# Performance work log

Hardware: AMD Instinct MI355X
Metric: run time of the kernel (lower is better)

The kernel has to match this reference:

```python
import jax, jax.numpy as jnp
import numpy as np

H = 2048          # hidden_size
E = 8             # num_experts
TOPK = 2          # num_experts_per_tok
I = 1408          # moe_intermediate_size
IS = 5632         # shared_expert_intermediate_size


def setup_inputs() -> dict:
    key = jax.random.key(0)
    ks = jax.random.split(key, 10)
    s = 0.02
    return {
        "hidden_states": jax.random.normal(ks[0], (2, 512, H), dtype=jnp.float32),
        "gate_w": jax.random.normal(ks[1], (H, E), dtype=jnp.float32) * s,
        "wg": jax.random.normal(ks[2], (E, H, I), dtype=jnp.float32) * s,
        "wu": jax.random.normal(ks[3], (E, H, I), dtype=jnp.float32) * s,
        "wd": jax.random.normal(ks[4], (E, I, H), dtype=jnp.float32) * s,
        "sg": jax.random.normal(ks[5], (H, IS), dtype=jnp.float32) * s,
        "su": jax.random.normal(ks[6], (H, IS), dtype=jnp.float32) * s,
        "sd": jax.random.normal(ks[7], (IS, H), dtype=jnp.float32) * s,
        "shared_gate_w": jax.random.normal(ks[8], (H, 1), dtype=jnp.float32) * s,
    }


def reference(hidden_states, gate_w, wg, wu, wd, sg, su, sd, shared_gate_w):
    B, S, Hd = hidden_states.shape
    x = hidden_states.reshape(-1, Hd)                       # [T, H]
    # Router (softmax in fp32, as in the torch code)
    router_logits = x @ gate_w                              # [T, E]
    probs = jax.nn.softmax(router_logits.astype(jnp.float32), axis=-1)
    rw, sel = jax.lax.top_k(probs, TOPK)                    # [T, K]
    # norm_topk_prob = False -> no renormalization
    rw = rw.astype(x.dtype)
    # Dense combine weights: w[t,e] = sum_k rw[t,k] * 1[sel[t,k]==e]
    combine = (jax.nn.one_hot(sel, E, dtype=x.dtype) * rw[..., None]).sum(axis=1)  # [T, E]
    # Per-expert SwiGLU MLP over all tokens, zero-weighted where unselected
    g = jnp.einsum('th,ehi->eti', x, wg)                    # [E, T, I]
    u = jnp.einsum('th,ehi->eti', x, wu)                    # [E, T, I]
    y = jnp.einsum('eti,eih->eth', jax.nn.silu(g) * u, wd)  # [E, T, H]
    moe_out = jnp.einsum('eth,te->th', y, combine)          # [T, H]
    # Shared expert with sigmoid gate
    shared = (jax.nn.silu(x @ sg) * (x @ su)) @ sd          # [T, H]
    shared = jax.nn.sigmoid(x @ shared_gate_w) * shared     # [T, H]
    final = moe_out + shared
    return final.reshape(B, S, Hd), router_logits
```

## Files before the change

kernel.cpp:

```cpp
#include <hip/hip_runtime.h>
#include <cstdint>
#include <cstddef>

#define Tn 1024
#define Hn 2048
#define En 8
#define In 1408
#define ISn 5632

typedef __attribute__((ext_vector_type(8))) short bf16x8;
typedef __attribute__((ext_vector_type(4))) float f32x4;

__device__ __forceinline__ unsigned short f2bf(float f) {
  unsigned u = __builtin_bit_cast(unsigned, f);
  u += 0x7fffu + ((u >> 16) & 1u);
  return (unsigned short)(u >> 16);
}

#define PK2(a, b) ((unsigned)f2bf(a) | ((unsigned)f2bf(b) << 16))
#define SWZ(row, bir) (((row) << 7) | ((((bir) >> 4) ^ ((row) & 7)) << 4) | ((bir) & 15))

__global__ void router_kernel(const float* __restrict__ x, const float* __restrict__ gw,
                              const float* __restrict__ sgw, float* __restrict__ logits_out,
                              float* __restrict__ combine, float* __restrict__ sgate) {
  int t = blockIdx.x;
  int l = threadIdx.x;
  const float* xr = x + (size_t)t * Hn;
  float acc[En];
#pragma unroll
  for (int e = 0; e < En; ++e) acc[e] = 0.f;
  float accs = 0.f;
  for (int h = l; h < Hn; h += 64) {
    float xv = xr[h];
    const float4 g0 = *(const float4*)(gw + (size_t)h * En);
    const float4 g1 = *(const float4*)(gw + (size_t)h * En + 4);
    acc[0] += xv * g0.x; acc[1] += xv * g0.y; acc[2] += xv * g0.z; acc[3] += xv * g0.w;
    acc[4] += xv * g1.x; acc[5] += xv * g1.y; acc[6] += xv * g1.z; acc[7] += xv * g1.w;
    accs += xv * sgw[h];
  }
#pragma unroll
  for (int e = 0; e < En; ++e) {
#pragma unroll
    for (int off = 32; off > 0; off >>= 1) acc[e] += __shfl_down(acc[e], off);
  }
#pragma unroll
  for (int off = 32; off > 0; off >>= 1) accs += __shfl_down(accs, off);
  if (l == 0) {
    float mx = acc[0];
#pragma unroll
    for (int e = 1; e < En; ++e) mx = fmaxf(mx, acc[e]);
    float p[En], s = 0.f;
#pragma unroll
    for (int e = 0; e < En; ++e) { p[e] = expf(acc[e] - mx); s += p[e]; }
    float inv = 1.f / s;
#pragma unroll
    for (int e = 0; e < En; ++e) p[e] *= inv;
    int i1 = 0;
#pragma unroll
    for (int e = 1; e < En; ++e) if (p[e] > p[i1]) i1 = e;
    int i2 = (i1 == 0) ? 1 : 0;
#pragma unroll
    for (int e = 0; e < En; ++e) if (e != i1 && p[e] > p[i2]) i2 = e;
#pragma unroll
    for (int e = 0; e < En; ++e)
      combine[t * En + e] = (e == i1 || e == i2) ? p[e] : 0.f;
    sgate[t] = 1.f / (1.f + expf(-accs));
#pragma unroll
    for (int e = 0; e < En; ++e) logits_out[t * En + e] = acc[e];
  }
}

__global__ void cvt_x_kernel(const float* __restrict__ x, unsigned short* __restrict__ xb) {
  int i = (blockIdx.x * 256 + threadIdx.x) << 2;
  float4 v = *(const float4*)(x + i);
  ushort4 o;
  o.x = f2bf(v.x); o.y = f2bf(v.y); o.z = f2bf(v.z); o.w = f2bf(v.w);
  *(ushort4*)(xb + i) = o;
}

__device__ __forceinline__ void stage_b(char* sB, const float* __restrict__ src, int ldb, int tid) {
  const int kb = tid >> 5;
  const int nb = tid & 31;
  const float* p = src + (size_t)(kb * 8) * ldb + nb * 4;
  float4 r0 = *(const float4*)p; p += ldb;
  float4 r1 = *(const float4*)p; p += ldb;
  float4 r2 = *(const float4*)p; p += ldb;
  float4 r3 = *(const float4*)p; p += ldb;
  float4 r4 = *(const float4*)p; p += ldb;
  float4 r5 = *(const float4*)p; p += ldb;
  float4 r6 = *(const float4*)p; p += ldb;
  float4 r7 = *(const float4*)p;
  uint4 pk;
  int n, off;
#define STORE_ROW(J, F)                                                        \
  n = nb * 4 + (J);                                                            \
  pk.x = PK2(r0.F, r1.F); pk.y = PK2(r2.F, r3.F);                              \
  pk.z = PK2(r4.F, r5.F); pk.w = PK2(r6.F, r7.F);                              \
  off = (n << 7) | (((kb ^ (n & 7)) << 4));                                    \
  *(uint4*)(sB + off) = pk;
  STORE_ROW(0, x)
  STORE_ROW(1, y)
  STORE_ROW(2, z)
  STORE_ROW(3, w)
#undef STORE_ROW
}

__global__ __launch_bounds__(256, 2)
void gateup_kernel(const unsigned short* __restrict__ xb,
                   const float* __restrict__ Wg, const float* __restrict__ Wu,
                   const float* __restrict__ combine, const float* __restrict__ sgate,
                   unsigned short* __restrict__ actout, int N, int mode) {
  __shared__ char smem[48 * 1024];
  char* sA = smem;
  char* sBg = smem + 16 * 1024;
  char* sBu = smem + 32 * 1024;

  const int tid = threadIdx.x;
  const int lane = tid & 63;
  const int wid = tid >> 6;
  const int wm = wid >> 1, wn = wid & 1;
  const int e = blockIdx.y;
  const int ntiles = N >> 7;
  const int mt = blockIdx.x / ntiles;
  const int nt = blockIdx.x - mt * ntiles;
  const int m0 = mt << 7, n0 = nt << 7;

  const float* Bg0 = Wg + (size_t)e * Hn * N + n0;
  const float* Bu0 = Wu + (size_t)e * Hn * N + n0;
  unsigned short* aout = actout + (size_t)e * Tn * N;

  f32x4 accg[4][4], accu[4][4];
#pragma unroll
  for (int i = 0; i < 4; ++i)
#pragma unroll
    for (int j = 0; j < 4; ++j) {
      accg[i][j] = {0.f, 0.f, 0.f, 0.f};
      accu[i][j] = {0.f, 0.f, 0.f, 0.f};
    }

  for (int kt = 0; kt < Hn / 64; ++kt) {
    const int k0 = kt << 6;
#pragma unroll
    for (int q = 0; q < 4; ++q) {
      int cc = tid + (q << 8);
      int row = cc >> 3, c = cc & 7;
      uint4 v = *(const uint4*)(xb + (size_t)(m0 + row) * Hn + k0 + (c << 3));
      *(uint4*)(sA + SWZ(row, c << 4)) = v;
    }
    stage_b(sBg, Bg0 + (size_t)k0 * N, N, tid);
    stage_b(sBu, Bu0 + (size_t)k0 * N, N, tid);
    __syncthreads();
#pragma unroll
    for (int kk = 0; kk < 2; ++kk) {
      bf16x8 af[4], bg[4], bu[4];
      const int bir = (kk << 6) + ((lane >> 4) << 4);
#pragma unroll
      for (int mi = 0; mi < 4; ++mi) {
        int row = (wm << 6) + (mi << 4) + (lane & 15);
        af[mi] = *(const bf16x8*)(sA + SWZ(row, bir));
      }
#pragma unroll
      for (int ni = 0; ni < 4; ++ni) {
        int n = (wn << 6) + (ni << 4) + (lane & 15);
        bg[ni] = *(const bf16x8*)(sBg + SWZ(n, bir));
        bu[ni] = *(const bf16x8*)(sBu + SWZ(n, bir));
      }
#pragma unroll
      for (int mi = 0; mi < 4; ++mi)
#pragma unroll
        for (int ni = 0; ni < 4; ++ni) {
          accg[mi][ni] = __builtin_amdgcn_mfma_f32_16x16x32_bf16(af[mi], bg[ni], accg[mi][ni], 0, 0, 0);
          accu[mi][ni] = __builtin_amdgcn_mfma_f32_16x16x32_bf16(af[mi], bu[ni], accu[mi][ni], 0, 0, 0);
        }
    }
    __syncthreads();
  }

#pragma unroll
  for (int mi = 0; mi < 4; ++mi)
#pragma unroll
    for (int ni = 0; ni < 4; ++ni)
#pragma unroll
      for (int r = 0; r < 4; ++r) {
        int m = m0 + (wm << 6) + (mi << 4) + ((lane >> 4) << 2) + r;
        int n = n0 + (wn << 6) + (ni << 4) + (lane & 15);
        float sc = (mode == 0) ? combine[(m << 3) + e] : sgate[m];
        float g = accg[mi][ni][r];
        float u = accu[mi][ni][r];
        float val = sc * (g / (1.f + __expf(-g))) * u;
        aout[(size_t)m * N + n] = f2bf(val);
      }
}

__global__ __launch_bounds__(256, 2)
void down_kernel(const unsigned short* __restrict__ act, const unsigned short* __restrict__ acts,
                 const float* __restrict__ wd, const float* __restrict__ sd,
                 float* __restrict__ out) {
  __shared__ char smem[32 * 1024];
  char* sA = smem;
  char* sB = smem + 16 * 1024;

  const int tid = threadIdx.x;
  const int lane = tid & 63;
  const int wid = tid >> 6;
  const int wm = wid >> 1, wn = wid & 1;
  const int mt = blockIdx.x >> 4, nt = blockIdx.x & 15;
  const int m0 = mt << 7, n0 = nt << 7;
  const int ktBeg = blockIdx.y * 132, ktEnd = ktBeg + 132;

  f32x4 acc[4][4];
#pragma unroll
  for (int i = 0; i < 4; ++i)
#pragma unroll
    for (int j = 0; j < 4; ++j) acc[i][j] = {0.f, 0.f, 0.f, 0.f};

  for (int kt = ktBeg; kt < ktEnd; ++kt) {
    const int k0 = kt << 6;
    const unsigned short* aSrc;
    const float* bSrc;
    int lda;
    if (k0 < En * In) {
      int ex = k0 / In;
      int i0 = k0 - ex * In;
      aSrc = act + ((size_t)ex * Tn + m0) * In + i0;
      lda = In;
      bSrc = wd + ((size_t)ex * In + i0) * Hn + n0;
    } else {
      int j0 = k0 - En * In;
      aSrc = acts + (size_t)m0 * ISn + j0;
      lda = ISn;
      bSrc = sd + (size_t)j0 * Hn + n0;
    }
#pragma unroll
    for (int q = 0; q < 4; ++q) {
      int cc = tid + (q << 8);
      int row = cc >> 3, c = cc & 7;
      uint4 v = *(const uint4*)(aSrc + (size_t)row * lda + (c << 3));
      *(uint4*)(sA + SWZ(row, c << 4)) = v;
    }
    stage_b(sB, bSrc, Hn, tid);
    __syncthreads();
#pragma unroll
    for (int kk = 0; kk < 2; ++kk) {
      bf16x8 af[4], bf[4];
      const int bir = (kk << 6) + ((lane >> 4) << 4);
#pragma unroll
      for (int mi = 0; mi < 4; ++mi) {
        int row = (wm << 6) + (mi << 4) + (lane & 15);
        af[mi] = *(const bf16x8*)(sA + SWZ(row, bir));
      }
#pragma unroll
      for (int ni = 0; ni < 4; ++ni) {
        int n = (wn << 6) + (ni << 4) + (lane & 15);
        bf[ni] = *(const bf16x8*)(sB + SWZ(n, bir));
      }
#pragma unroll
      for (int mi = 0; mi < 4; ++mi)
#pragma unroll
        for (int ni = 0; ni < 4; ++ni)
          acc[mi][ni] = __builtin_amdgcn_mfma_f32_16x16x32_bf16(af[mi], bf[ni], acc[mi][ni], 0, 0, 0);
    }
    __syncthreads();
  }

#pragma unroll
  for (int mi = 0; mi < 4; ++mi)
#pragma unroll
    for (int ni = 0; ni < 4; ++ni)
#pragma unroll
      for (int r = 0; r < 4; ++r) {
        int m = m0 + (wm << 6) + (mi << 4) + ((lane >> 4) << 2) + r;
        int n = n0 + (wn << 6) + (ni << 4) + (lane & 15);
        atomicAdd(out + (size_t)m * Hn + n, acc[mi][ni][r]);
      }
}

extern "C" void kernel_launch(void* const* d_in, const int* in_sizes, int n_in,
                              void* d_out, int out_size, void* d_ws, size_t ws_size,
                              hipStream_t stream) {
  const float* x   = (const float*)d_in[0];
  const float* gw  = (const float*)d_in[1];
  const float* wg  = (const float*)d_in[2];
  const float* wu  = (const float*)d_in[3];
  const float* wd  = (const float*)d_in[4];
  const float* sg  = (const float*)d_in[5];
  const float* su  = (const float*)d_in[6];
  const float* sd  = (const float*)d_in[7];
  const float* sgw = (const float*)d_in[8];
  float* out = (float*)d_out;
  float* logits_out = out + (size_t)Tn * Hn;

  char* w = (char*)d_ws;
  float* combine = (float*)w;
  float* sgate = combine + Tn * En;
  unsigned short* xb   = (unsigned short*)(w + 64 * 1024);
  unsigned short* actE = xb + (size_t)Tn * Hn;
  unsigned short* actS = actE + (size_t)En * Tn * In;

  hipMemsetAsync(d_out, 0, (size_t)out_size * sizeof(float), stream);
  router_kernel<<<Tn, 64, 0, stream>>>(x, gw, sgw, logits_out, combine, sgate);
  cvt_x_kernel<<<(Tn * Hn / 4) / 256, 256, 0, stream>>>(x, xb);
  gateup_kernel<<<dim3(8 * (In / 128), En), 256, 0, stream>>>(xb, wg, wu, combine, sgate, actE, In, 0);
  gateup_kernel<<<dim3(8 * (ISn / 128), 1), 256, 0, stream>>>(xb, sg, su, combine, sgate, actS, ISn, 1);
  down_kernel<<<dim3(128, 2), 256, 0, stream>>>(actE, actS, wd, sd, out);
}
```

Measured before the change: 888.3 us.

## Route tokens per expert and compute only selected tokens in MoE GEMMs

The router now builds per-expert token lists and weights with atomics, replacing dense combine weights. The expert gate/up and down GEMMs gather only the routed tokens and skip empty M-tiles, which should cut expert compute roughly fourfold. Expert results are scattered back to the output with float atomics, and the shared-expert down projection gets its own split-K kernel. The change also alters the LDS swizzle to XOR in higher row bits, adds atomic contention, and makes summation order nondeterministic.

```diff
diff --git a/kernel.cpp b/kernel.cpp
--- a/kernel.cpp
+++ b/kernel.cpp
@@ -18,11 +18,13 @@
 }
 
 #define PK2(a, b) ((unsigned)f2bf(a) | ((unsigned)f2bf(b) << 16))
-#define SWZ(row, bir) (((row) << 7) | ((((bir) >> 4) ^ ((row) & 7)) << 4) | ((bir) & 15))
+#define SWZC(row, kc) (((kc) ^ ((row) & 7) ^ (((row) >> 3) & 7)) & 7)
+#define SWZ(row, bir) (((row) << 7) | (SWZC((row), ((bir) >> 4)) << 4) | ((bir) & 15))
 
 __global__ void router_kernel(const float* __restrict__ x, const float* __restrict__ gw,
                               const float* __restrict__ sgw, float* __restrict__ logits_out,
-                              float* __restrict__ combine, float* __restrict__ sgate) {
+                              float* __restrict__ sgate, int* __restrict__ tokList,
+                              float* __restrict__ wgt, int* __restrict__ cnt) {
   int t = blockIdx.x;
   int l = threadIdx.x;
   const float* xr = x + (size_t)t * Hn;
@@ -61,9 +63,10 @@
     int i2 = (i1 == 0) ? 1 : 0;
 #pragma unroll
     for (int e = 0; e < En; ++e) if (e != i1 && p[e] > p[i2]) i2 = e;
-#pragma unroll
-    for (int e = 0; e < En; ++e)
-      combine[t * En + e] = (e == i1 || e == i2) ? p[e] : 0.f;
+    int p1 = atomicAdd(&cnt[i1], 1);
+    tokList[(i1 << 10) + p1] = t; wgt[(i1 << 10) + p1] = p[i1];
+    int p2 = atomicAdd(&cnt[i2], 1);
+    tokList[(i2 << 10) + p2] = t; wgt[(i2 << 10) + p2] = p[i2];
     sgate[t] = 1.f / (1.f + expf(-accs));
 #pragma unroll
     for (int e = 0; e < En; ++e) logits_out[t * En + e] = acc[e];
@@ -96,7 +99,7 @@
   n = nb * 4 + (J);                                                            \
   pk.x = PK2(r0.F, r1.F); pk.y = PK2(r2.F, r3.F);                              \
   pk.z = PK2(r4.F, r5.F); pk.w = PK2(r6.F, r7.F);                              \
-  off = (n << 7) | (((kb ^ (n & 7)) << 4));                                    \
+  off = (n << 7) | (SWZC(n, kb) << 4);                                         \
   *(uint4*)(sB + off) = pk;
   STORE_ROW(0, x)
   STORE_ROW(1, y)
@@ -108,8 +111,15 @@
 __global__ __launch_bounds__(256, 2)
 void gateup_kernel(const unsigned short* __restrict__ xb,
                    const float* __restrict__ Wg, const float* __restrict__ Wu,
-                   const float* __restrict__ combine, const float* __restrict__ sgate,
+                   const float* __restrict__ wgt, const float* __restrict__ sgate,
+                   const int* __restrict__ tokList, const int* __restrict__ cnt,
                    unsigned short* __restrict__ actout, int N, int mode) {
+  const int e = blockIdx.y;
+  const int nt = blockIdx.x >> 3, mt = blockIdx.x & 7;
+  const int cntE = (mode == 0) ? cnt[e] : Tn;
+  const int m0 = mt << 7, n0 = nt << 7;
+  if (m0 >= cntE) return;
+
   __shared__ char smem[48 * 1024];
   char* sA = smem;
   char* sBg = smem + 16 * 1024;
@@ -119,16 +129,24 @@
   const int lane = tid & 63;
   const int wid = tid >> 6;
   const int wm = wid >> 1, wn = wid & 1;
-  const int e = blockIdx.y;
-  const int ntiles = N >> 7;
-  const int mt = blockIdx.x / ntiles;
-  const int nt = blockIdx.x - mt * ntiles;
-  const int m0 = mt << 7, n0 = nt << 7;
 
   const float* Bg0 = Wg + (size_t)e * Hn * N + n0;
   const float* Bu0 = Wu + (size_t)e * Hn * N + n0;
   unsigned short* aout = actout + (size_t)e * Tn * N;
 
+  int tokq[4];
+#pragma unroll
+  for (int q = 0; q < 4; ++q) {
+    int row = (tid + (q << 8)) >> 3;
+    int m = m0 + row;
+    if (mode == 0) {
+      int mc = m < cntE ? m : cntE - 1;
+      tokq[q] = tokList[(e << 10) + mc];
+    } else {
+      tokq[q] = m;
+    }
+  }
+
   f32x4 accg[4][4], accu[4][4];
 #pragma unroll
   for (int i = 0; i < 4; ++i)
@@ -144,7 +162,7 @@
     for (int q = 0; q < 4; ++q) {
       int cc = tid + (q << 8);
       int row = cc >> 3, c = cc & 7;
-      uint4 v = *(const uint4*)(xb + (size_t)(m0 + row) * Hn + k0 + (c << 3));
+      uint4 v = *(const uint4*)(xb + (size_t)tokq[q] * Hn + k0 + (c << 3));
       *(uint4*)(sA + SWZ(row, c << 4)) = v;
     }
     stage_b(sBg, Bg0 + (size_t)k0 * N, N, tid);
@@ -184,18 +202,25 @@
       for (int r = 0; r < 4; ++r) {
         int m = m0 + (wm << 6) + (mi << 4) + ((lane >> 4) << 2) + r;
         int n = n0 + (wn << 6) + (ni << 4) + (lane & 15);
-        float sc = (mode == 0) ? combine[(m << 3) + e] : sgate[m];
-        float g = accg[mi][ni][r];
-        float u = accu[mi][ni][r];
-        float val = sc * (g / (1.f + __expf(-g))) * u;
-        aout[(size_t)m * N + n] = f2bf(val);
+        if (m < cntE) {
+          float sc = (mode == 0) ? wgt[(e << 10) + m] : sgate[m];
+          float g = accg[mi][ni][r];
+          float u = accu[mi][ni][r];
+          aout[(size_t)m * N + n] = f2bf(sc * (g / (1.f + __expf(-g))) * u);
+        }
       }
 }
 
 __global__ __launch_bounds__(256, 2)
-void down_kernel(const unsigned short* __restrict__ act, const unsigned short* __restrict__ acts,
-                 const float* __restrict__ wd, const float* __restrict__ sd,
-                 float* __restrict__ out) {
+void down_e_kernel(const unsigned short* __restrict__ act, const float* __restrict__ wd,
+                   const int* __restrict__ tokList, const int* __restrict__ cnt,
+                   float* __restrict__ out) {
+  const int e = blockIdx.y;
+  const int nt = blockIdx.x >> 3, mt = blockIdx.x & 7;
+  const int cntE = cnt[e];
+  const int m0 = mt << 7, n0 = nt << 7;
+  if (m0 >= cntE) return;
+
   __shared__ char smem[32 * 1024];
   char* sA = smem;
   char* sB = smem + 16 * 1024;
@@ -204,9 +229,9 @@
   const int lane = tid & 63;
   const int wid = tid >> 6;
   const int wm = wid >> 1, wn = wid & 1;
-  const int mt = blockIdx.x >> 4, nt = blockIdx.x & 15;
-  const int m0 = mt << 7, n0 = nt << 7;
-  const int ktBeg = blockIdx.y * 132, ktEnd = ktBeg + 132;
+
+  const unsigned short* aBase = act + ((size_t)e * Tn + m0) * In;
+  const float* bBase = wd + (size_t)e * In * Hn + n0;
 
   f32x4 acc[4][4];
 #pragma unroll
@@ -214,31 +239,87 @@
 #pragma unroll
     for (int j = 0; j < 4; ++j) acc[i][j] = {0.f, 0.f, 0.f, 0.f};
 
-  for (int kt = ktBeg; kt < ktEnd; ++kt) {
+  for (int kt = 0; kt < In / 64; ++kt) {
     const int k0 = kt << 6;
-    const unsigned short* aSrc;
-    const float* bSrc;
-    int lda;
-    if (k0 < En * In) {
-      int ex = k0 / In;
-      int i0 = k0 - ex * In;
-      aSrc = act + ((size_t)ex * Tn + m0) * In + i0;
-      lda = In;
-      bSrc = wd + ((size_t)ex * In + i0) * Hn + n0;
-    } else {
-      int j0 = k0 - En * In;
-      aSrc = acts + (size_t)m0 * ISn + j0;
-      lda = ISn;
-      bSrc = sd + (size_t)j0 * Hn + n0;
-    }
 #pragma unroll
     for (int q = 0; q < 4; ++q) {
       int cc = tid + (q << 8);
       int row = cc >> 3, c = cc & 7;
-      uint4 v = *(const uint4*)(aSrc + (size_t)row * lda + (c << 3));
+      uint4 v = *(const uint4*)(aBase + (size_t)row * In + k0 + (c << 3));
       *(uint4*)(sA + SWZ(row, c << 4)) = v;
     }
-    stage_b(sB, bSrc, Hn, tid);
+    stage_b(sB, bBase + (size_t)k0 * Hn, Hn, tid);
+    __syncthreads();
+#pragma unroll
+    for (int kk = 0; kk < 2; ++kk) {
+      bf16x8 af[4], bf[4];
+      const int bir = (kk << 6) + ((lane >> 4) << 4);
+#pragma unroll
+      for (int mi = 0; mi < 4; ++mi) {
+        int row = (wm << 6) + (mi << 4) + (lane & 15);
+        af[mi] = *(const bf16x8*)(sA + SWZ(row, bir));
+      }
+#pragma unroll
+      for (int ni = 0; ni < 4; ++ni) {
+        int n = (wn << 6) + (ni << 4) + (lane & 15);
+        bf[ni] = *(const bf16x8*)(sB + SWZ(n, bir));
+      }
+#pragma unroll
+      for (int mi = 0; mi < 4; ++mi)
+#pragma unroll
+        for (int ni = 0; ni < 4; ++ni)
+          acc[mi][ni] = __builtin_amdgcn_mfma_f32_16x16x32_bf16(af[mi], bf[ni], acc[mi][ni], 0, 0, 0);
+    }
+    __syncthreads();
+  }
+
+#pragma unroll
+  for (int mi = 0; mi < 4; ++mi)
+#pragma unroll
+    for (int ni = 0; ni < 4; ++ni)
+#pragma unroll
+      for (int r = 0; r < 4; ++r) {
+        int m = m0 + (wm << 6) + (mi << 4) + ((lane >> 4) << 2) + r;
+        int n = n0 + (wn << 6) + (ni << 4) + (lane & 15);
+        if (m < cntE) {
+          int tok = tokList[(e << 10) + m];
+          atomicAdd(out + (size_t)tok * Hn + n, acc[mi][ni][r]);
+        }
+      }
+}
+
+__global__ __launch_bounds__(256, 2)
+void down_s_kernel(const unsigned short* __restrict__ acts, const float* __restrict__ sd,
+                   float* __restrict__ out) {
+  const int nt = blockIdx.x >> 3, mt = blockIdx.x & 7;
+  const int m0 = mt << 7, n0 = nt << 7;
+  const int ktBeg = blockIdx.y * 44, ktEnd = ktBeg + 44;
+
+  __shared__ char smem[32 * 1024];
+  char* sA = smem;
+  char* sB = smem + 16 * 1024;
+
+  const int tid = threadIdx.x;
+  const int lane = tid & 63;
+  const int wid = tid >> 6;
+  const int wm = wid >> 1, wn = wid & 1;
+
+  f32x4 acc[4][4];
+#pragma unroll
+  for (int i = 0; i < 4; ++i)
+#pragma unroll
+    for (int j = 0; j < 4; ++j) acc[i][j] = {0.f, 0.f, 0.f, 0.f};
+
+  for (int kt = ktBeg; kt < ktEnd; ++kt) {
+    const int k0 = kt << 6;
+#pragma unroll
+    for (int q = 0; q < 4; ++q) {
+      int cc = tid + (q << 8);
+      int row = cc >> 3, c = cc & 7;
+      uint4 v = *(const uint4*)(acts + (size_t)(m0 + row) * ISn + k0 + (c << 3));
+      *(uint4*)(sA + SWZ(row, c << 4)) = v;
+    }
+    stage_b(sB, sd + (size_t)k0 * Hn + n0, Hn, tid);
     __syncthreads();
 #pragma unroll
     for (int kk = 0; kk < 2; ++kk) {
@@ -291,16 +372,20 @@
   float* logits_out = out + (size_t)Tn * Hn;
 
   char* w = (char*)d_ws;
-  float* combine = (float*)w;
-  float* sgate = combine + Tn * En;
-  unsigned short* xb   = (unsigned short*)(w + 64 * 1024);
+  int*   cnt     = (int*)w;
+  float* sgate   = (float*)(w + 4096);
+  int*   tokList = (int*)(w + 8192);
+  float* wgt     = (float*)(w + 40960);
+  unsigned short* xb   = (unsigned short*)(w + 131072);
   unsigned short* actE = xb + (size_t)Tn * Hn;
   unsigned short* actS = actE + (size_t)En * Tn * In;
 
   hipMemsetAsync(d_out, 0, (size_t)out_size * sizeof(float), stream);
-  router_kernel<<<Tn, 64, 0, stream>>>(x, gw, sgw, logits_out, combine, sgate);
+  hipMemsetAsync(cnt, 0, En * sizeof(int), stream);
+  router_kernel<<<Tn, 64, 0, stream>>>(x, gw, sgw, logits_out, sgate, tokList, wgt, cnt);
   cvt_x_kernel<<<(Tn * Hn / 4) / 256, 256, 0, stream>>>(x, xb);
-  gateup_kernel<<<dim3(8 * (In / 128), En), 256, 0, stream>>>(xb, wg, wu, combine, sgate, actE, In, 0);
-  gateup_kernel<<<dim3(8 * (ISn / 128), 1), 256, 0, stream>>>(xb, sg, su, combine, sgate, actS, ISn, 1);
-  down_kernel<<<dim3(128, 2), 256, 0, stream>>>(actE, actS, wd, sd, out);
-}
+  gateup_kernel<<<dim3((In / 128) * 8, En), 256, 0, stream>>>(xb, wg, wu, wgt, sgate, tokList, cnt, actE, In, 0);
+  gateup_kernel<<<dim3((ISn / 128) * 8, 1), 256, 0, stream>>>(xb, sg, su, wgt, sgate, tokList, cnt, actS, ISn, 1);
+  down_e_kernel<<<dim3(16 * 8, En), 256, 0, stream>>>(actE, wd, tokList, cnt, out);
+  down_s_kernel<<<dim3(16 * 8, 2), 256, 0, stream>>>(actS, sd, out);
+}
```

After: 904.3 us. About the same (+1.8%).
